# Optimization experiments

Hardware: AMD Instinct MI355X
Metric: run time of the kernel (lower is better)

Reference implementation:

```python
import jax, jax.numpy as jnp
import numpy as np

B, T, C = 4, 4096, 256
H = 4
D = C // H
EPS = 1e-5


def layer_norm(x, w, b):
    mean = x.mean(axis=-1, keepdims=True)
    var = x.var(axis=-1, keepdims=True)
    return w * (x - mean) / jnp.sqrt(var + EPS) + b


def setup_inputs() -> dict:
    key = jax.random.key(0)
    ks = jax.random.split(key, 8)
    s = lambda n: 1.0 / np.sqrt(n)
    return {
        "x": jax.random.normal(ks[0], (B, T, C), jnp.float32),
        "qkv_w": jax.random.normal(ks[1], (C, 3 * C), jnp.float32) * s(C),
        "qkv_b": jnp.zeros((3 * C,), jnp.float32),
        "proj_w": jax.random.normal(ks[2], (C, C), jnp.float32) * s(C),
        "proj_b": jnp.zeros((C,), jnp.float32),
        "n1_w": jnp.ones((C,), jnp.float32),
        "n1_b": jnp.zeros((C,), jnp.float32),
        "ffn_w1": jax.random.normal(ks[3], (C, 3 * C), jnp.float32) * s(C),
        "ffn_b1": jnp.zeros((3 * C,), jnp.float32),
        "ffn_w2": jax.random.normal(ks[4], (3 * C, C), jnp.float32) * s(3 * C),
        "ffn_b2": jnp.zeros((C,), jnp.float32),
        "n2_w": jnp.ones((C,), jnp.float32),
        "n2_b": jnp.zeros((C,), jnp.float32),
    }


def reference(x, qkv_w, qkv_b, proj_w, proj_b, n1_w, n1_b,
              ffn_w1, ffn_b1, ffn_w2, ffn_b2, n2_w, n2_b):
    scale = D ** -0.5
    qkv = (x @ qkv_w + qkv_b).reshape(B, T, 3, H, D)
    qkv = jnp.transpose(qkv, (2, 0, 3, 1, 4))  # [3, B, H, T, D]
    q, k, v = qkv[0], qkv[1], qkv[2]
    attn = jnp.einsum('bhtd,bhsd->bhts', q, k) * scale  # [B,H,T,T]
    attn = jax.nn.softmax(attn, axis=-1)
    out = jnp.einsum('bhts,bhsd->bhtd', attn, v)
    out = jnp.transpose(out, (0, 2, 1, 3)).reshape(B, T, C)
    attn_out = out @ proj_w + proj_b
    x = layer_norm(x + attn_out, n1_w, n1_b)
    h = jax.nn.gelu(x @ ffn_w1 + ffn_b1, approximate=False)
    ffn_out = h @ ffn_w2 + ffn_b2
    x = layer_norm(x + ffn_out, n2_w, n2_b)
    return x
```

## Files before the change

kernel.cpp:

```cpp
#include <hip/hip_runtime.h>
#include <cstdint>
#include <cstddef>

typedef __bf16 bf16;
typedef __bf16 bf16x8 __attribute__((ext_vector_type(8)));
typedef __bf16 bf16x4 __attribute__((ext_vector_type(4)));
typedef _Float16 f16;
typedef _Float16 f16x4 __attribute__((ext_vector_type(4)));
typedef _Float16 f16x8 __attribute__((ext_vector_type(8)));
typedef __fp16 fp16x2 __attribute__((ext_vector_type(2)));
typedef float f32x4 __attribute__((ext_vector_type(4)));

#define DEV static __device__ __forceinline__
#if __has_builtin(__builtin_amdgcn_exp2f)
#define EXP2(x) __builtin_amdgcn_exp2f(x)
#else
#define EXP2(x) exp2f(x)
#endif
#define QSCALE 0.18033688011112042f

DEV float gelu_exact(float v) {
  return 0.5f * v * (1.0f + erff(v * 0.70710678118654752f));
}

template <int ROWS>
DEV void stage_swz(bf16* lbase, const bf16* g, int ldK) {
  const int tid = threadIdx.x;
  const int wave = tid >> 6, lane = tid & 63;
  const int r8 = lane >> 3;
  const int c = (lane & 7) ^ r8;
  const size_t goff = (size_t)r8 * ldK + c * 8;
#pragma unroll
  for (int ch = wave; ch < (ROWS >> 3); ch += 4) {
    __builtin_amdgcn_global_load_lds(
        (const __attribute__((address_space(1))) void*)(g + (size_t)ch * 8 * ldK + goff),
        (__attribute__((address_space(3))) void*)(lbase + ch * 512), 16, 0, 0);
  }
}

DEV int swzi(int R, int c) { return R * 64 + ((c ^ (R & 7)) << 3); }

__global__ void cvt_w_kernel(const float* __restrict__ qkv_w, bf16* __restrict__ qwt,
                             const float* __restrict__ proj_w, bf16* __restrict__ pwt,
                             const float* __restrict__ f1w, bf16* __restrict__ f1wt,
                             const float* __restrict__ f2w, bf16* __restrict__ f2wt,
                             const float* __restrict__ x, bf16* __restrict__ xb) {
  int blk = blockIdx.x;
  const int tid = threadIdx.x;
  if (blk >= 160) {
    const size_t i = ((size_t)(blk - 160) * 256 + tid) * 8;
    const float4 a0 = *(const float4*)(x + i);
    const float4 a1 = *(const float4*)(x + i + 4);
    bf16x8 v;
    v[0] = (bf16)a0.x; v[1] = (bf16)a0.y; v[2] = (bf16)a0.z; v[3] = (bf16)a0.w;
    v[4] = (bf16)a1.x; v[5] = (bf16)a1.y; v[6] = (bf16)a1.z; v[7] = (bf16)a1.w;
    *(bf16x8*)(xb + i) = v;
    return;
  }
  const float* w; bf16* o; int K, N;
  if (blk < 48)       { w = qkv_w;  o = qwt;  K = 256; N = 768; }
  else if (blk < 64)  { w = proj_w; o = pwt;  K = 256; N = 256; blk -= 48; }
  else if (blk < 112) { w = f1w;    o = f1wt; K = 256; N = 768; blk -= 64; }
  else                { w = f2w;    o = f2wt; K = 768; N = 256; blk -= 112; }
  const int ntiles = N >> 6;
  const int kt = blk / ntiles, nt = blk - kt * ntiles;
  const int k0 = kt * 64, n0 = nt * 64;
  __shared__ float tile[64][65];
#pragma unroll
  for (int j = 0; j < 4; ++j) {
    const int c = j * 256 + tid;
    const int row = c >> 4, c4 = (c & 15) * 4;
    const float4 v = *(const float4*)(w + (size_t)(k0 + row) * N + n0 + c4);
    tile[row][c4] = v.x; tile[row][c4 + 1] = v.y;
    tile[row][c4 + 2] = v.z; tile[row][c4 + 3] = v.w;
  }
  __syncthreads();
#pragma unroll
  for (int j = 0; j < 4; ++j) {
    const int c = j * 256 + tid;
    const int n = c >> 4, k4 = (c & 15) * 4;
    bf16x4 ov;
#pragma unroll
    for (int i = 0; i < 4; ++i) ov[i] = (bf16)tile[k4 + i][n];
    *(bf16x4*)(o + (size_t)(n0 + n) * K + k0 + k4) = ov;
  }
}

__global__ __launch_bounds__(256, 3)
void gemm_qkv_kernel(const bf16* __restrict__ A, const bf16* __restrict__ Wt,
                     const float* __restrict__ bias, bf16* __restrict__ qb,
                     bf16* __restrict__ kb, f16* __restrict__ vt) {
  const int tid = threadIdx.x;
  const int wave = tid >> 6, lane = tid & 63;
  const int quad = lane >> 4, l15 = lane & 15;
  const int m0 = blockIdx.y * 128, n0 = blockIdx.x * 128;
  const int mw = (wave >> 1) * 64, nw = (wave & 1) * 64;
  const int K = 256;

  __shared__ __align__(16) char smem[128 * 132 * 2];
  bf16* lA = (bf16*)smem;
  bf16* lB = lA + 128 * 64;

  f32x4 acc[4][4] = {};

  for (int k0 = 0; k0 < K; k0 += 64) {
    stage_swz<128>(lA, A + (size_t)m0 * K + k0, K);
    stage_swz<128>(lB, Wt + (size_t)n0 * K + k0, K);
    __syncthreads();
#pragma unroll
    for (int ks = 0; ks < 2; ++ks) {
      bf16x8 af[4], bfm[4];
#pragma unroll
      for (int i = 0; i < 4; ++i)
        af[i] = *(const bf16x8*)(lA + swzi(mw + i * 16 + l15, ks * 4 + quad));
#pragma unroll
      for (int j = 0; j < 4; ++j)
        bfm[j] = *(const bf16x8*)(lB + swzi(nw + j * 16 + l15, ks * 4 + quad));
#pragma unroll
      for (int i = 0; i < 4; ++i)
#pragma unroll
        for (int j = 0; j < 4; ++j)
          acc[i][j] = __builtin_amdgcn_mfma_f32_16x16x32_bf16(af[i], bfm[j],
                                                              acc[i][j], 0, 0, 0);
    }
    __syncthreads();
  }

  const int b = m0 >> 12, trow = m0 & 4095;
  const bool isV = (n0 >= 512);
  float bv[4];
#pragma unroll
  for (int j = 0; j < 4; ++j) bv[j] = bias[n0 + nw + 16 * j + l15];

  if (isV) {
    f16* ET = (f16*)smem;
#pragma unroll
    for (int i = 0; i < 4; ++i)
#pragma unroll
      for (int j = 0; j < 4; ++j) {
        const int n = nw + 16 * j + l15, t = mw + 16 * i + quad * 4;
        f16x4 hv;
#pragma unroll
        for (int r = 0; r < 4; ++r) hv[r] = (f16)(acc[i][j][r] + bv[j]);
        *(f16x4*)(ET + n * 132 + t) = hv;
      }
    __syncthreads();
    const int nr = tid >> 4, l4 = tid & 15;
    const int g32 = l4 >> 2, q8 = l4 & 3;
#pragma unroll
    for (int pass = 0; pass < 8; ++pass) {
      const int n = pass * 16 + nr;
      const int gn = n0 + n;
      const int h = (gn >> 6) & 3, d = gn & 63;
      const f16* srcr = ET + n * 132 + g32 * 32 + q8 * 4;
      const f16x4 lo = *(const f16x4*)(srcr);
      const f16x4 hi = *(const f16x4*)(srcr + 16);
      union { f16x4 h4[2]; f16x8 h8; } u;
      u.h4[0] = lo; u.h4[1] = hi;
      *(f16x8*)(vt + ((size_t)(b * 4 + h) * 64 + d) * 4096 + trow + l4 * 8) =
          u.h8;
    }
  } else {
    const bool isQ = (n0 < 256);
    const float sc = isQ ? QSCALE : 1.0f;
    bf16* ET = (bf16*)smem;
#pragma unroll
    for (int i = 0; i < 4; ++i)
#pragma unroll
      for (int j = 0; j < 4; ++j) {
        const int n = nw + 16 * j + l15;
#pragma unroll
        for (int r = 0; r < 4; ++r) {
          const int t = mw + 16 * i + quad * 4 + r;
          ET[t * 132 + n] = (bf16)((acc[i][j][r] + bv[j]) * sc);
        }
      }
    __syncthreads();
    bf16* qk = isQ ? qb : kb;
    const int nr = tid >> 4, l4 = tid & 15;
    const int gn = n0 + l4 * 8;
    const int h = (gn >> 6) & 3, d = gn & 63;
#pragma unroll
    for (int pass = 0; pass < 8; ++pass) {
      const int t = pass * 16 + nr;
      const bf16x4 lo = *(const bf16x4*)(ET + t * 132 + l4 * 8);
      const bf16x4 hi = *(const bf16x4*)(ET + t * 132 + l4 * 8 + 4);
      union { bf16x4 h4[2]; bf16x8 h8; } u;
      u.h4[0] = lo; u.h4[1] = hi;
      *(bf16x8*)(qk + ((size_t)(b * 4 + h) * 4096 + trow + t) * 64 + d) = u.h8;
    }
  }
}

__global__ __launch_bounds__(256, 2)
void attn_kernel(const bf16* __restrict__ q, const bf16* __restrict__ k,
                 const f16* __restrict__ vt, bf16* __restrict__ o0,
                 bf16* __restrict__ o1, float* __restrict__ pD) {
  const int tid = threadIdx.x;
  const int wave = tid >> 6, lane = tid & 63;
  const int quad = lane >> 4, l15 = lane & 15;
  const int bh = blockIdx.y;
  const int q0 = blockIdx.x * 128;
  const int z = blockIdx.z;
  const int kvbase = z * 2048;
  __shared__ bf16 lK[2][64 * 64];
  __shared__ f16  lV[2][64 * 64];

  bf16x8 qa0[2], qa1[2];
#pragma unroll
  for (int s = 0; s < 2; ++s) {
    const bf16* qp =
        q + ((size_t)bh * 4096 + q0 + wave * 32 + s * 16 + l15) * 64 + quad * 8;
    qa0[s] = *(const bf16x8*)(qp);
    qa1[s] = *(const bf16x8*)(qp + 32);
  }

  const int srow = lane >> 3;
  const int sc = (lane & 7) ^ srow;
  const bf16* kbase = k + ((size_t)bh * 4096 + kvbase) * 64;
  const f16*  vbase = vt + (size_t)bh * 64 * 4096 + kvbase;

#define STAGE_KV(buf, it_)                                                     \
  {                                                                            \
    const bf16* ks_ = kbase + (size_t)(it_) * 4096;                            \
    const f16*  vs_ = vbase + (it_) * 64;                                      \
    _Pragma("unroll")                                                          \
    for (int i_ = 0; i_ < 2; ++i_) {                                           \
      const int r0_ = i_ * 32 + wave * 8;                                      \
      __builtin_amdgcn_global_load_lds(                                        \
          (const __attribute__((address_space(1))) void*)(                     \
              ks_ + (size_t)(r0_ + srow) * 64 + sc * 8),                       \
          (__attribute__((address_space(3))) void*)(lK[buf] + r0_ * 64),       \
          16, 0, 0);                                                           \
      __builtin_amdgcn_global_load_lds(                                        \
          (const __attribute__((address_space(1))) void*)(                     \
              vs_ + (size_t)(r0_ + srow) * 4096 + sc * 8),                     \
          (__attribute__((address_space(3))) void*)(lV[buf] + r0_ * 64),       \
          16, 0, 0);                                                           \
    }                                                                          \
  }

  STAGE_KV(0, 0);

  f32x4 accO[2][4] = {};
  f32x4 accD[2] = {};
  const f16x8 vone8 = {(f16)1.0f, (f16)1.0f, (f16)1.0f, (f16)1.0f,
                       (f16)1.0f, (f16)1.0f, (f16)1.0f, (f16)1.0f};

  for (int it = 0; it < 32; ++it) {
    const int cur = it & 1;
    __syncthreads();
    if (it + 1 < 32) STAGE_KV(cur ^ 1, it + 1);

    f32x4 sf[2][4];
    __builtin_amdgcn_s_setprio(1);
#pragma unroll
    for (int c = 0; c < 4; ++c) {
      const bf16x8 kb0 = *(const bf16x8*)(lK[cur] + swzi(c * 16 + l15, quad));
      const bf16x8 kb1 = *(const bf16x8*)(lK[cur] + swzi(c * 16 + l15, 4 + quad));
#pragma unroll
      for (int s = 0; s < 2; ++s) {
        f32x4 t = {};
        t = __builtin_amdgcn_mfma_f32_16x16x32_bf16(kb0, qa0[s], t, 0, 0, 0);
        t = __builtin_amdgcn_mfma_f32_16x16x32_bf16(kb1, qa1[s], t, 0, 0, 0);
        sf[s][c] = t;
      }
    }
    __builtin_amdgcn_s_setprio(0);

    f16x8 pa[2][2];
#pragma unroll
    for (int s = 0; s < 2; ++s)
#pragma unroll
      for (int c2 = 0; c2 < 2; ++c2) {
        union { fp16x2 h2[4]; f16x8 h8; } u;
        u.h2[0] = __builtin_amdgcn_cvt_pkrtz(EXP2(sf[s][2 * c2][0]),
                                             EXP2(sf[s][2 * c2][1]));
        u.h2[1] = __builtin_amdgcn_cvt_pkrtz(EXP2(sf[s][2 * c2][2]),
                                             EXP2(sf[s][2 * c2][3]));
        u.h2[2] = __builtin_amdgcn_cvt_pkrtz(EXP2(sf[s][2 * c2 + 1][0]),
                                             EXP2(sf[s][2 * c2 + 1][1]));
        u.h2[3] = __builtin_amdgcn_cvt_pkrtz(EXP2(sf[s][2 * c2 + 1][2]),
                                             EXP2(sf[s][2 * c2 + 1][3]));
        pa[s][c2] = u.h8;
      }

    __builtin_amdgcn_s_setprio(1);
#pragma unroll
    for (int s = 0; s < 2; ++s)
#pragma unroll
      for (int c2 = 0; c2 < 2; ++c2)
        accD[s] = __builtin_amdgcn_mfma_f32_16x16x32_f16(pa[s][c2], vone8,
                                                         accD[s], 0, 0, 0);

#pragma unroll
    for (int c2 = 0; c2 < 2; ++c2) {
#pragma unroll
      for (int n = 0; n < 4; ++n) {
        const f16x8 vb =
            *(const f16x8*)(lV[cur] + swzi(n * 16 + l15, c2 * 4 + quad));
#pragma unroll
        for (int s = 0; s < 2; ++s)
          accO[s][n] = __builtin_amdgcn_mfma_f32_16x16x32_f16(pa[s][c2], vb,
                                                              accO[s][n], 0, 0, 0);
      }
    }
    __builtin_amdgcn_s_setprio(0);
  }
#undef STAGE_KV

  bf16* po = z ? o1 : o0;
  const int b = bh >> 2, h = bh & 3;
#pragma unroll
  for (int s = 0; s < 2; ++s) {
    float inv[4];
#pragma unroll
    for (int r = 0; r < 4; ++r) inv[r] = 1.0f / accD[s][r];
#pragma unroll
    for (int r = 0; r < 4; ++r) {
      const int t = q0 + wave * 32 + s * 16 + quad * 4 + r;
      if (l15 == 0) pD[(size_t)(z * 16 + bh) * 4096 + t] = accD[s][r];
#pragma unroll
      for (int n = 0; n < 4; ++n)
        po[(size_t)(b * 4096 + t) * 256 + h * 64 + n * 16 + l15] =
            (bf16)(accO[s][n][r] * inv[r]);
    }
  }
}

__global__ __launch_bounds__(256, 3)
void gemm_ffn1_kernel(const bf16* __restrict__ A, const bf16* __restrict__ Wt,
                      const float* __restrict__ bias, bf16* __restrict__ ob) {
  const int tid = threadIdx.x;
  const int wave = tid >> 6, lane = tid & 63;
  const int quad = lane >> 4, l15 = lane & 15;
  const int m0 = blockIdx.y * 128, n0 = blockIdx.x * 128;
  const int mw = (wave >> 1) * 64, nw = (wave & 1) * 64;
  const int K = 256;

  __shared__ bf16 lA[128 * 64];
  __shared__ bf16 lB[128 * 64];

  f32x4 acc[4][4] = {};

  for (int k0 = 0; k0 < K; k0 += 64) {
    stage_swz<128>(lA, A + (size_t)m0 * K + k0, K);
    stage_swz<128>(lB, Wt + (size_t)n0 * K + k0, K);
    __syncthreads();
#pragma unroll
    for (int ks = 0; ks < 2; ++ks) {
      bf16x8 af[4], bfm[4];
#pragma unroll
      for (int i = 0; i < 4; ++i)
        af[i] = *(const bf16x8*)(lA + swzi(mw + i * 16 + l15, ks * 4 + quad));
#pragma unroll
      for (int j = 0; j < 4; ++j)
        bfm[j] = *(const bf16x8*)(lB + swzi(nw + j * 16 + l15, ks * 4 + quad));
#pragma unroll
      for (int i = 0; i < 4; ++i)
#pragma unroll
        for (int j = 0; j < 4; ++j)
          acc[i][j] = __builtin_amdgcn_mfma_f32_16x16x32_bf16(af[i], bfm[j],
                                                              acc[i][j], 0, 0, 0);
    }
    __syncthreads();
  }

#pragma unroll
  for (int i = 0; i < 4; ++i) {
#pragma unroll
    for (int j = 0; j < 4; ++j) {
      const int n = n0 + nw + j * 16 + l15;
      const float bs = bias[n];
#pragma unroll
      for (int r = 0; r < 4; ++r) {
        const int m = m0 + mw + i * 16 + quad * 4 + r;
        ob[(size_t)m * 768 + n] = (bf16)gelu_exact(acc[i][j][r] + bs);
      }
    }
  }
}

template <int KTILES, bool COMBINE, bool RESID_BF16, bool WRITE_F, bool WRITE_B>
__global__ __launch_bounds__(256, 3)
void gemm_ln_kernel(const bf16* __restrict__ A, const bf16* __restrict__ A2,
                    const float* __restrict__ pD, const bf16* __restrict__ Wt,
                    const float* __restrict__ bias, const void* __restrict__ Rv,
                    const float* __restrict__ lw, const float* __restrict__ lb,
                    float* __restrict__ outf, bf16* __restrict__ outb) {
  const int tid = threadIdx.x;
  const int wave = tid >> 6, lane = tid & 63;
  const int quad = lane >> 4, l15 = lane & 15;
  const int m0 = blockIdx.x * 32;
  const int nw = wave * 64;
  const int K = KTILES * 64;
  __shared__ bf16 lA[32 * 64];
  __shared__ bf16 lB[256 * 64];
  __shared__ float lnsum[4][32];
  __shared__ float lnsq[4][32];
  __shared__ float lnstat[32][2];
  f32x4 acc[2][4] = {};

  for (int kt = 0; kt < KTILES; ++kt) {
    const int k0 = kt * 64;
    if constexpr (COMBINE) {
      const int row = tid >> 3, cc = tid & 7;
      const int am = m0 + row;
      const int h = (k0 + cc * 8) >> 6;
      const int ab = am >> 12, at = am & 4095;
      const float d0 = pD[(size_t)(ab * 4 + h) * 4096 + at];
      const float d1 = pD[(size_t)(16 + ab * 4 + h) * 4096 + at];
      const float wsum = 1.0f / (d0 + d1);
      const float w0 = d0 * wsum, w1 = d1 * wsum;
      const bf16x8 a0 = *(const bf16x8*)(A  + (size_t)am * K + k0 + cc * 8);
      const bf16x8 a1 = *(const bf16x8*)(A2 + (size_t)am * K + k0 + cc * 8);
      bf16x8 cv;
#pragma unroll
      for (int i = 0; i < 8; ++i)
        cv[i] = (bf16)((float)a0[i] * w0 + (float)a1[i] * w1);
      *(bf16x8*)(lA + swzi(row, cc)) = cv;
    } else {
      stage_swz<32>(lA, A + (size_t)m0 * K + k0, K);
    }
    stage_swz<256>(lB, Wt + k0, K);
    __syncthreads();
#pragma unroll
    for (int ks = 0; ks < 2; ++ks) {
      bf16x8 af[2], bfm[4];
#pragma unroll
      for (int i = 0; i < 2; ++i)
        af[i] = *(const bf16x8*)(lA + swzi(i * 16 + l15, ks * 4 + quad));
#pragma unroll
      for (int j = 0; j < 4; ++j)
        bfm[j] = *(const bf16x8*)(lB + swzi(nw + j * 16 + l15, ks * 4 + quad));
#pragma unroll
      for (int i = 0; i < 2; ++i)
#pragma unroll
        for (int j = 0; j < 4; ++j)
          acc[i][j] = __builtin_amdgcn_mfma_f32_16x16x32_bf16(af[i], bfm[j],
                                                              acc[i][j], 0, 0, 0);
    }
    __syncthreads();
  }

  float bv[4], lwv[4], lbv[4];
#pragma unroll
  for (int j = 0; j < 4; ++j) {
    const int col = nw + 16 * j + l15;
    bv[j] = bias[col]; lwv[j] = lw[col]; lbv[j] = lb[col];
  }
#pragma unroll
  for (int i = 0; i < 2; ++i) {
    float ps[4] = {}, pq[4] = {};
#pragma unroll
    for (int j = 0; j < 4; ++j) {
#pragma unroll
      for (int r = 0; r < 4; ++r) {
        const int m = m0 + 16 * i + 4 * quad + r;
        const size_t ri = (size_t)m * 256 + nw + 16 * j + l15;
        const float rv = RESID_BF16 ? (float)((const bf16*)Rv)[ri]
                                    : ((const float*)Rv)[ri];
        const float v = acc[i][j][r] + bv[j] + rv;
        acc[i][j][r] = v;
        ps[r] += v;
        pq[r] += v * v;
      }
    }
#pragma unroll
    for (int r = 0; r < 4; ++r) {
#pragma unroll
      for (int mm = 1; mm < 16; mm <<= 1) {
        ps[r] += __shfl_xor(ps[r], mm, 64);
        pq[r] += __shfl_xor(pq[r], mm, 64);
      }
      if (l15 == 0) {
        lnsum[wave][16 * i + 4 * quad + r] = ps[r];
        lnsq[wave][16 * i + 4 * quad + r] = pq[r];
      }
    }
  }
  __syncthreads();
  if (tid < 32) {
    const float s = lnsum[0][tid] + lnsum[1][tid] + lnsum[2][tid] + lnsum[3][tid];
    const float sq = lnsq[0][tid] + lnsq[1][tid] + lnsq[2][tid] + lnsq[3][tid];
    const float mean = s * (1.0f / 256.0f);
    const float var = sq * (1.0f / 256.0f) - mean * mean;
    lnstat[tid][0] = mean;
    lnstat[tid][1] = rsqrtf(var + 1e-5f);
  }
  __syncthreads();
#pragma unroll
  for (int i = 0; i < 2; ++i) {
#pragma unroll
    for (int r = 0; r < 4; ++r) {
      const int row = 16 * i + 4 * quad + r;
      const float mean = lnstat[row][0], rstd = lnstat[row][1];
#pragma unroll
      for (int j = 0; j < 4; ++j) {
        const float ov = (acc[i][j][r] - mean) * rstd * lwv[j] + lbv[j];
        const size_t gi = (size_t)(m0 + row) * 256 + nw + 16 * j + l15;
        if constexpr (WRITE_F) outf[gi] = ov;
        if constexpr (WRITE_B) outb[gi] = (bf16)ov;
      }
    }
  }
}

extern "C" void kernel_launch(void* const* d_in, const int* in_sizes, int n_in,
                              void* d_out, int out_size, void* d_ws, size_t ws_size,
                              hipStream_t stream) {
  const float* x      = (const float*)d_in[0];
  const float* qkv_w  = (const float*)d_in[1];
  const float* qkv_b  = (const float*)d_in[2];
  const float* proj_w = (const float*)d_in[3];
  const float* proj_b = (const float*)d_in[4];
  const float* n1_w   = (const float*)d_in[5];
  const float* n1_b   = (const float*)d_in[6];
  const float* ffn_w1 = (const float*)d_in[7];
  const float* ffn_b1 = (const float*)d_in[8];
  const float* ffn_w2 = (const float*)d_in[9];
  const float* ffn_b2 = (const float*)d_in[10];
  const float* n2_w   = (const float*)d_in[11];
  const float* n2_b   = (const float*)d_in[12];
  float* out = (float*)d_out;

  char* ws = (char*)d_ws;
  bf16*  qwt  = (bf16*)(ws + 0);
  bf16*  pwt  = (bf16*)(ws + 393216);
  bf16*  f1wt = (bf16*)(ws + 524288);
  bf16*  f2wt = (bf16*)(ws + 917504);
  bf16*  qb   = (bf16*)(ws + 1310720);
  bf16*  kb   = (bf16*)(ws + 9699328);
  f16*   vtb  = (f16*)(ws + 18087936);
  bf16*  attn = (bf16*)(ws + 26476544);
  bf16*  x1b  = (bf16*)(ws + 34865152);
  bf16*  hbuf = (bf16*)(ws + 1310720);
  bf16*  xb   = (bf16*)(ws + 34865152);
  bf16*  po1  = (bf16*)(ws + 43253760);
  float* pden = (float*)(ws + 51642368);

  cvt_w_kernel<<<2208, 256, 0, stream>>>(qkv_w, qwt, proj_w, pwt,
                                         ffn_w1, f1wt, ffn_w2, f2wt, x, xb);
  gemm_qkv_kernel<<<dim3(6, 128), 256, 0, stream>>>(xb, qwt, qkv_b, qb, kb, vtb);
  attn_kernel<<<dim3(32, 16, 2), 256, 0, stream>>>(qb, kb, vtb, attn, po1, pden);
  gemm_ln_kernel<4, true, false, false, true><<<512, 256, 0, stream>>>(
      attn, po1, pden, pwt, proj_b, x, n1_w, n1_b, nullptr, x1b);
  gemm_ffn1_kernel<<<dim3(6, 128), 256, 0, stream>>>(x1b, f1wt, ffn_b1, hbuf);
  gemm_ln_kernel<12, false, true, true, false><<<512, 256, 0, stream>>>(
      hbuf, nullptr, nullptr, f2wt, ffn_b2, x1b, n2_w, n2_b, out, nullptr);
}
```

Baseline: 233.0 us.

## Fuse proj+LN1 GEMM with FFN1 GEMM+GELU in one kernel

Merges the attention projection + residual + LayerNorm kernel with the first FFN GEMM + GELU. The normalized 32-row tile stays in LDS as the A operand for FFN1, which removes a kernel launch and the x1b re-read. The fused kernel still writes x1b for the later residual. In exchange, FFN1 now runs with 32-row tiles that restage the full weight per block, uses more LDS with launch bounds lowered to 2, and its inner loops are not unrolled, which may reduce MFMA efficiency compared with the 128x128 tiles it replaces.

```diff
diff --git a/kernel.cpp b/kernel.cpp
--- a/kernel.cpp
+++ b/kernel.cpp
@@ -328,36 +328,57 @@
   }
 }
 
-__global__ __launch_bounds__(256, 3)
-void gemm_ffn1_kernel(const bf16* __restrict__ A, const bf16* __restrict__ Wt,
-                      const float* __restrict__ bias, bf16* __restrict__ ob) {
+__global__ __launch_bounds__(256, 2)
+void ln1_ffn1_kernel(const bf16* __restrict__ A, const bf16* __restrict__ A2,
+                     const float* __restrict__ pD, const bf16* __restrict__ pwt,
+                     const float* __restrict__ pb, const float* __restrict__ xres,
+                     const float* __restrict__ lw, const float* __restrict__ lb,
+                     bf16* __restrict__ x1b, const bf16* __restrict__ f1wt,
+                     const float* __restrict__ f1b, bf16* __restrict__ ob) {
   const int tid = threadIdx.x;
   const int wave = tid >> 6, lane = tid & 63;
   const int quad = lane >> 4, l15 = lane & 15;
-  const int m0 = blockIdx.y * 128, n0 = blockIdx.x * 128;
-  const int mw = (wave >> 1) * 64, nw = (wave & 1) * 64;
-  const int K = 256;
-
-  __shared__ bf16 lA[128 * 64];
-  __shared__ bf16 lB[128 * 64];
-
-  f32x4 acc[4][4] = {};
-
-  for (int k0 = 0; k0 < K; k0 += 64) {
-    stage_swz<128>(lA, A + (size_t)m0 * K + k0, K);
-    stage_swz<128>(lB, Wt + (size_t)n0 * K + k0, K);
+  const int m0 = blockIdx.x * 32;
+  const int nw = wave * 64;
+  __shared__ bf16 lA[32 * 64];
+  __shared__ bf16 lB[256 * 64];
+  __shared__ bf16 aT[4 * 32 * 64];
+  __shared__ float lnsum[4][32];
+  __shared__ float lnsq[4][32];
+  __shared__ float lnstat[32][2];
+  f32x4 acc[2][4] = {};
+
+  for (int kt = 0; kt < 4; ++kt) {
+    const int k0 = kt * 64;
+    {
+      const int row = tid >> 3, cc = tid & 7;
+      const int am = m0 + row;
+      const int ab = am >> 12, at = am & 4095;
+      const float d0 = pD[(size_t)(ab * 4 + kt) * 4096 + at];
+      const float d1 = pD[(size_t)(16 + ab * 4 + kt) * 4096 + at];
+      const float wsum = 1.0f / (d0 + d1);
+      const float w0 = d0 * wsum, w1 = d1 * wsum;
+      const bf16x8 a0 = *(const bf16x8*)(A  + (size_t)am * 256 + k0 + cc * 8);
+      const bf16x8 a1 = *(const bf16x8*)(A2 + (size_t)am * 256 + k0 + cc * 8);
+      bf16x8 cv;
+#pragma unroll
+      for (int i = 0; i < 8; ++i)
+        cv[i] = (bf16)((float)a0[i] * w0 + (float)a1[i] * w1);
+      *(bf16x8*)(lA + swzi(row, cc)) = cv;
+    }
+    stage_swz<256>(lB, pwt + k0, 256);
     __syncthreads();
 #pragma unroll
     for (int ks = 0; ks < 2; ++ks) {
-      bf16x8 af[4], bfm[4];
-#pragma unroll
-      for (int i = 0; i < 4; ++i)
-        af[i] = *(const bf16x8*)(lA + swzi(mw + i * 16 + l15, ks * 4 + quad));
+      bf16x8 af[2], bfm[4];
+#pragma unroll
+      for (int i = 0; i < 2; ++i)
+        af[i] = *(const bf16x8*)(lA + swzi(i * 16 + l15, ks * 4 + quad));
 #pragma unroll
       for (int j = 0; j < 4; ++j)
         bfm[j] = *(const bf16x8*)(lB + swzi(nw + j * 16 + l15, ks * 4 + quad));
 #pragma unroll
-      for (int i = 0; i < 4; ++i)
+      for (int i = 0; i < 2; ++i)
 #pragma unroll
         for (int j = 0; j < 4; ++j)
           acc[i][j] = __builtin_amdgcn_mfma_f32_16x16x32_bf16(af[i], bfm[j],
@@ -366,25 +387,121 @@
     __syncthreads();
   }
 
-#pragma unroll
-  for (int i = 0; i < 4; ++i) {
+  float bv[4], lwv[4], lbv[4];
+#pragma unroll
+  for (int j = 0; j < 4; ++j) {
+    const int col = nw + 16 * j + l15;
+    bv[j] = pb[col]; lwv[j] = lw[col]; lbv[j] = lb[col];
+  }
+#pragma unroll
+  for (int i = 0; i < 2; ++i) {
+    float ps[4] = {}, pq[4] = {};
 #pragma unroll
     for (int j = 0; j < 4; ++j) {
-      const int n = n0 + nw + j * 16 + l15;
-      const float bs = bias[n];
 #pragma unroll
       for (int r = 0; r < 4; ++r) {
-        const int m = m0 + mw + i * 16 + quad * 4 + r;
-        ob[(size_t)m * 768 + n] = (bf16)gelu_exact(acc[i][j][r] + bs);
-      }
-    }
-  }
-}
-
-template <int KTILES, bool COMBINE, bool RESID_BF16, bool WRITE_F, bool WRITE_B>
+        const int m = m0 + 16 * i + 4 * quad + r;
+        const size_t ri = (size_t)m * 256 + nw + 16 * j + l15;
+        const float v = acc[i][j][r] + bv[j] + xres[ri];
+        acc[i][j][r] = v;
+        ps[r] += v;
+        pq[r] += v * v;
+      }
+    }
+#pragma unroll
+    for (int r = 0; r < 4; ++r) {
+#pragma unroll
+      for (int mm = 1; mm < 16; mm <<= 1) {
+        ps[r] += __shfl_xor(ps[r], mm, 64);
+        pq[r] += __shfl_xor(pq[r], mm, 64);
+      }
+      if (l15 == 0) {
+        lnsum[wave][16 * i + 4 * quad + r] = ps[r];
+        lnsq[wave][16 * i + 4 * quad + r] = pq[r];
+      }
+    }
+  }
+  __syncthreads();
+  if (tid < 32) {
+    const float s = lnsum[0][tid] + lnsum[1][tid] + lnsum[2][tid] + lnsum[3][tid];
+    const float sq = lnsq[0][tid] + lnsq[1][tid] + lnsq[2][tid] + lnsq[3][tid];
+    const float mean = s * (1.0f / 256.0f);
+    const float var = sq * (1.0f / 256.0f) - mean * mean;
+    lnstat[tid][0] = mean;
+    lnstat[tid][1] = rsqrtf(var + 1e-5f);
+  }
+  __syncthreads();
+#pragma unroll
+  for (int i = 0; i < 2; ++i) {
+#pragma unroll
+    for (int r = 0; r < 4; ++r) {
+      const int row = 16 * i + 4 * quad + r;
+      const float mean = lnstat[row][0], rstd = lnstat[row][1];
+#pragma unroll
+      for (int j = 0; j < 4; ++j) {
+        const float ov = (acc[i][j][r] - mean) * rstd * lwv[j] + lbv[j];
+        const bf16 obf = (bf16)ov;
+        const size_t gi = (size_t)(m0 + row) * 256 + nw + 16 * j + l15;
+        x1b[gi] = obf;
+        const int cg = 16 * j + l15;
+        aT[wave * 2048 + row * 64 + ((((cg >> 3) ^ (row & 7))) << 3) + (cg & 7)]
+            = obf;
+      }
+    }
+  }
+  __syncthreads();
+
+  const int nwB = wave * 32;
+#pragma unroll 1
+  for (int nt = 0; nt < 6; ++nt) {
+    f32x4 acc2[2][2] = {};
+    const bf16* Bb = f1wt + (size_t)nt * 128 * 256;
+#pragma unroll 1
+    for (int kh = 0; kh < 2; ++kh) {
+      stage_swz<128>(lB,        Bb + kh * 128, 256);
+      stage_swz<128>(lB + 8192, Bb + kh * 128 + 64, 256);
+      __syncthreads();
+#pragma unroll
+      for (int kk = 0; kk < 2; ++kk) {
+        const bf16* aTk = aT + (kh * 2 + kk) * 2048;
+        const bf16* lbk = lB + kk * 8192;
+#pragma unroll
+        for (int ks = 0; ks < 2; ++ks) {
+          bf16x8 af[2], bfm[2];
+#pragma unroll
+          for (int i = 0; i < 2; ++i)
+            af[i] = *(const bf16x8*)(aTk + swzi(i * 16 + l15, ks * 4 + quad));
+#pragma unroll
+          for (int j = 0; j < 2; ++j)
+            bfm[j] = *(const bf16x8*)(lbk + swzi(nwB + j * 16 + l15, ks * 4 + quad));
+#pragma unroll
+          for (int i = 0; i < 2; ++i)
+#pragma unroll
+            for (int j = 0; j < 2; ++j)
+              acc2[i][j] = __builtin_amdgcn_mfma_f32_16x16x32_bf16(
+                  af[i], bfm[j], acc2[i][j], 0, 0, 0);
+        }
+      }
+      __syncthreads();
+    }
+#pragma unroll
+    for (int j = 0; j < 2; ++j) {
+      const int gn = nt * 128 + nwB + 16 * j + l15;
+      const float bs = f1b[gn];
+#pragma unroll
+      for (int i = 0; i < 2; ++i)
+#pragma unroll
+        for (int r = 0; r < 4; ++r) {
+          const int m = m0 + 16 * i + quad * 4 + r;
+          ob[(size_t)m * 768 + gn] = (bf16)gelu_exact(acc2[i][j][r] + bs);
+        }
+    }
+  }
+}
+
+template <int KTILES, bool RESID_BF16, bool WRITE_F, bool WRITE_B>
 __global__ __launch_bounds__(256, 3)
-void gemm_ln_kernel(const bf16* __restrict__ A, const bf16* __restrict__ A2,
-                    const float* __restrict__ pD, const bf16* __restrict__ Wt,
+void gemm_ln_kernel(const bf16* __restrict__ A, const bf16* __restrict__ Wt,
                     const float* __restrict__ bias, const void* __restrict__ Rv,
                     const float* __restrict__ lw, const float* __restrict__ lb,
                     float* __restrict__ outf, bf16* __restrict__ outb) {
@@ -403,25 +520,7 @@
 
   for (int kt = 0; kt < KTILES; ++kt) {
     const int k0 = kt * 64;
-    if constexpr (COMBINE) {
-      const int row = tid >> 3, cc = tid & 7;
-      const int am = m0 + row;
-      const int h = (k0 + cc * 8) >> 6;
-      const int ab = am >> 12, at = am & 4095;
-      const float d0 = pD[(size_t)(ab * 4 + h) * 4096 + at];
-      const float d1 = pD[(size_t)(16 + ab * 4 + h) * 4096 + at];
-      const float wsum = 1.0f / (d0 + d1);
-      const float w0 = d0 * wsum, w1 = d1 * wsum;
-      const bf16x8 a0 = *(const bf16x8*)(A  + (size_t)am * K + k0 + cc * 8);
-      const bf16x8 a1 = *(const bf16x8*)(A2 + (size_t)am * K + k0 + cc * 8);
-      bf16x8 cv;
-#pragma unroll
-      for (int i = 0; i < 8; ++i)
-        cv[i] = (bf16)((float)a0[i] * w0 + (float)a1[i] * w1);
-      *(bf16x8*)(lA + swzi(row, cc)) = cv;
-    } else {
-      stage_swz<32>(lA, A + (size_t)m0 * K + k0, K);
-    }
+    stage_swz<32>(lA, A + (size_t)m0 * K + k0, K);
     stage_swz<256>(lB, Wt + k0, K);
     __syncthreads();
 #pragma unroll
@@ -543,9 +642,8 @@
                                          ffn_w1, f1wt, ffn_w2, f2wt, x, xb);
   gemm_qkv_kernel<<<dim3(6, 128), 256, 0, stream>>>(xb, qwt, qkv_b, qb, kb, vtb);
   attn_kernel<<<dim3(32, 16, 2), 256, 0, stream>>>(qb, kb, vtb, attn, po1, pden);
-  gemm_ln_kernel<4, true, false, false, true><<<512, 256, 0, stream>>>(
-      attn, po1, pden, pwt, proj_b, x, n1_w, n1_b, nullptr, x1b);
-  gemm_ffn1_kernel<<<dim3(6, 128), 256, 0, stream>>>(x1b, f1wt, ffn_b1, hbuf);
-  gemm_ln_kernel<12, false, true, true, false><<<512, 256, 0, stream>>>(
-      hbuf, nullptr, nullptr, f2wt, ffn_b2, x1b, n2_w, n2_b, out, nullptr);
-}
+  ln1_ffn1_kernel<<<512, 256, 0, stream>>>(attn, po1, pden, pwt, proj_b, x,
+                                           n1_w, n1_b, x1b, f1wt, ffn_b1, hbuf);
+  gemm_ln_kernel<12, true, true, false><<<512, 256, 0, stream>>>(
+      hbuf, f2wt, ffn_b2, x1b, n2_w, n2_b, out, nullptr);
+}
```

Measured after the change: 227.2 us, median of 2. 1.03x faster.
